# Kernel optimization log

Hardware: AMD Instinct MI355X
Metric: run time of the kernel (lower is better)

The kernel has to match this reference:

```python
import math
import jax, jax.numpy as jnp
import numpy as np

IMAGE_SIZE = 256
RADIUS = 10.0  # radius_list=[10.0] default
EYES_POS_LIST = [[-1, -1, -1], [-1, -1, 1], [-1, 1, -1], [-1, 1, 1],
                 [1, -1, -1], [1, -1, 1], [1, 1, -1], [1, 1, 1]]


def _pre_matrix(view_id):
    # projection_matrix @ look_at(eyes, 0, up=(0,0,1)), orthographic branch
    eyes = np.array(EYES_POS_LIST[view_id], np.float32)  # eyepos_scale=1.0
    ups = np.array([0.0, 0.0, 1.0], np.float32)
    z = eyes / max(float(np.linalg.norm(eyes)), 1e-6)
    x = np.cross(ups, z)
    x = x / max(float(np.linalg.norm(x)), 1e-6)
    y = np.cross(z, x)
    orient = np.eye(4, dtype=np.float32)
    orient[0, :3] = x
    orient[1, :3] = y
    orient[2, :3] = z
    trans = np.eye(4, dtype=np.float32)
    trans[:3, 3] = -eyes
    view = orient @ trans
    z_near, z_far = 0.1, 10.0
    proj = np.diag(np.array([1.5, 1.5, -2.0 / (z_far - z_near), 1.0], np.float32))
    proj[2, 3] = (z_far + z_near) / (z_far - z_near)
    return jnp.asarray((proj @ view).astype(np.float32))


def _p2i_max(pos_ij, feat, batch_inds, background, radius):
    """Splat each point onto its (i,j) pixel footprint with a cos kernel,
    reducing with max (background as init). pos_ij in NDC [-1,1]."""
    B, C, H, W = background.shape  # C == 1
    pts = (pos_ij * 0.5 + 0.5) * jnp.array([H - 1.0, W - 1.0], pos_ij.dtype)  # [P,2] pixel coords
    r = int(math.ceil(radius))
    offs = jnp.arange(-r, r + 2)  # cover full footprint around floor(center)
    di, dj = jnp.meshgrid(offs, offs, indexing="ij")
    di = di.reshape(-1)
    dj = dj.reshape(-1)  # [K], K=(2r+2)^2
    base = jnp.floor(pts).astype(jnp.int32)  # [P,2]
    pi = base[:, :1] + di[None, :]  # [P,K]
    pj = base[:, 1:] + dj[None, :]
    d = jnp.sqrt((pi.astype(pts.dtype) - pts[:, :1]) ** 2 +
                 (pj.astype(pts.dtype) - pts[:, 1:]) ** 2)
    w = jnp.where(d <= radius, jnp.cos(d * (jnp.pi / 2.0 / radius)), 0.0)  # cos kernel
    vals = w * feat  # feat [P,1] broadcasts -> [P,K]
    valid = (pi >= 0) & (pi < H) & (pj >= 0) & (pj < W)
    flat = batch_inds[:, None] * (H * W) + pi * W + pj
    flat = jnp.where(valid, flat, B * H * W)  # dump slot for out-of-bounds
    canvas = jnp.full((B * H * W + 1,), -jnp.inf, background.dtype)
    canvas = canvas.at[flat.reshape(-1)].max(vals.reshape(-1))
    return jnp.maximum(background, canvas[:-1].reshape(B, 1, H, W))


def _forward(data, view_id):
    B, N, _ = data.shape
    M = _pre_matrix(view_id)  # [4,4]
    pcd = data.reshape(-1, 3)  # [B*N,3]
    hom = pcd @ M[:, :3].T + M[:, 3][None, :]  # [B*N,4]
    xyz = hom[:, :3] / hom[:, 3:4]
    pos_ij = jnp.stack([-xyz[:, 1], xyz[:, 0]], axis=1)  # (i,j) = (-y, x)
    z = xyz[:, 2:3]
    feat = 1.0 - (z - z.min()) / (z.max() - z.min())  # [B*N,1]
    batch_inds = jnp.repeat(jnp.arange(B, dtype=jnp.int32), N)
    background = jnp.zeros((B, 1, IMAGE_SIZE, IMAGE_SIZE), data.dtype)
    return _p2i_max(pos_ij, feat, batch_inds, background, RADIUS)


def setup_inputs() -> dict:
    key = jax.random.key(0)
    data = jax.random.normal(key, (32, 4096, 3), dtype=jnp.float32) * 0.5  # unit-ish cloud
    return {"data": data, "view_id": 0}


def reference(data, view_id):
    return _forward(data, view_id)
```

## Files before the change

kernel.cpp:

```cpp
#include <hip/hip_runtime.h>
#include <math.h>

#define IMG_H 256
#define IMG_W 256
#define NBATCH 32
#define NPER 4096
#define NPTS (NBATCH * NPER)
#define STRIP 16
#define NSTRIPS (IMG_H / STRIP)
#define THREADS 1024
#define NWAVES (THREADS / 64)
#define PADL 19
#define ROWW 299
#define CANVAS_W (STRIP * ROWW)
#define KC  0.15707964f
#define KC3 0.47123890f
#define TMAX 2.4674011f
#define BBLK 64
#define CAP 2048


struct Mats { float m[8][12]; };

static void build_mats(float out[8][12]) {
  static const double EYES[8][3] = {
    {-1,-1,-1},{-1,-1, 1},{-1, 1,-1},{-1, 1, 1},
    { 1,-1,-1},{ 1,-1, 1},{ 1, 1,-1},{ 1, 1, 1}};
  for (int v = 0; v < 8; ++v) {
    const double* e = EYES[v];
    double en = sqrt(e[0]*e[0] + e[1]*e[1] + e[2]*e[2]);
    if (en < 1e-6) en = 1e-6;
    double z[3] = {e[0]/en, e[1]/en, e[2]/en};
    double x[3] = {-z[1], z[0], 0.0};
    double xn = sqrt(x[0]*x[0] + x[1]*x[1]);
    if (xn < 1e-6) xn = 1e-6;
    x[0] /= xn; x[1] /= xn; x[2] = 0.0;
    double y[3] = {z[1]*x[2] - z[2]*x[1],
                   z[2]*x[0] - z[0]*x[2],
                   z[0]*x[1] - z[1]*x[0]};
    const double s  = 1.5;
    const double pz = -2.0 / (10.0 - 0.1);
    const double c3 = (10.0 + 0.1) / (10.0 - 0.1);
    double dxe = x[0]*e[0] + x[1]*e[1] + x[2]*e[2];
    double dye = y[0]*e[0] + y[1]*e[1] + y[2]*e[2];
    double dze = z[0]*e[0] + z[1]*e[1] + z[2]*e[2];
    out[v][0] = (float)(s*x[0]); out[v][1] = (float)(s*x[1]);
    out[v][2] = (float)(s*x[2]); out[v][3] = (float)(-s*dxe);
    out[v][4] = (float)(s*y[0]); out[v][5] = (float)(s*y[1]);
    out[v][6] = (float)(s*y[2]); out[v][7] = (float)(-s*dye);
    out[v][8] = (float)(pz*z[0]); out[v][9] = (float)(pz*z[1]);
    out[v][10] = (float)(pz*z[2]); out[v][11] = (float)(-pz*dze + c3);
  }
}

__global__ __launch_bounds__(256)
void zminmax_part(const float* __restrict__ data,
                  const int* __restrict__ view_id,
                  Mats mats, float* __restrict__ red) {
  const int v = (*view_id) & 7;
  const float* M = mats.m[v];
  const float M8 = M[8], M9 = M[9], M10 = M[10], M11 = M[11];
  float zmin = INFINITY, zmax = -INFINITY;
  for (int p = blockIdx.x * blockDim.x + threadIdx.x; p < NPTS;
       p += BBLK * 256) {
    float x = data[3*p+0], y = data[3*p+1], zz = data[3*p+2];
    float z = M8*x + M9*y + M10*zz + M11;
    zmin = fminf(zmin, z);
    zmax = fmaxf(zmax, z);
  }
#pragma unroll
  for (int m = 32; m >= 1; m >>= 1) {
    zmin = fminf(zmin, __shfl_xor(zmin, m, 64));
    zmax = fmaxf(zmax, __shfl_xor(zmax, m, 64));
  }
  __shared__ float smn[4], smx[4];
  if ((threadIdx.x & 63) == 0) {
    smn[threadIdx.x >> 6] = zmin;
    smx[threadIdx.x >> 6] = zmax;
  }
  __syncthreads();
  if (threadIdx.x == 0) {
    float a = fminf(fminf(smn[0], smn[1]), fminf(smn[2], smn[3]));
    float b = fmaxf(fmaxf(smx[0], smx[1]), fmaxf(smx[2], smx[3]));
    red[blockIdx.x] = a;
    red[BBLK + blockIdx.x] = b;
  }
}

__global__ __launch_bounds__(THREADS, 8)
void splat_fused(const float* __restrict__ data,
                 const int* __restrict__ view_id,
                 Mats mats, const float* __restrict__ red,
                 float* __restrict__ out) {
  __shared__ unsigned int canvas[CANVAS_W];
  __shared__ float4 q4[CAP];
  __shared__ int qcnt;
  __shared__ float zred[2];

  const int tid  = threadIdx.x;
  const int lane = tid & 63;
  const int wid  = tid >> 6;
  const int b    = blockIdx.y;
  const int strip = (b < 16) ? (int)blockIdx.x : (15 - (int)blockIdx.x);
  const int si0  = strip * STRIP;

  const int v = (*view_id) & 7;
  const float* M = mats.m[v];
  const float M0 = M[0], M1 = M[1], M2 = M[2],  M3  = M[3];
  const float M4 = M[4], M5 = M[5], M6 = M[6],  M7  = M[7];
  const float M8 = M[8], M9 = M[9], M10 = M[10], M11 = M[11];

  for (int i = tid; i < CANVAS_W; i += THREADS) canvas[i] = 0u;
  if (tid < 64) {
    float a = fminf(red[tid], INFINITY);
    float c = fmaxf(red[BBLK + tid], -INFINITY);
#pragma unroll
    for (int m = 32; m >= 1; m >>= 1) {
      a = fminf(a, __shfl_xor(a, m, 64));
      c = fmaxf(c, __shfl_xor(c, m, 64));
    }
    if (tid == 0) { zred[0] = a; zred[1] = c; qcnt = 0; }
  }
  __syncthreads();

  const float zmin = zred[0];
  const float zinv = 1.0f / (zred[1] - zmin);

  const float2* src2 = (const float2*)(data + (size_t)b * NPER * 3);
#pragma unroll 1
  for (int chunk = 0; chunk < 2; ++chunk) {
    int f2base = chunk * 3072 + 3 * tid;
    float2 A = src2[f2base], Bv = src2[f2base + 1], Cv = src2[f2base + 2];
    float px[2] = {A.x, Bv.y};
    float py[2] = {A.y, Cv.x};
    float pw[2] = {Bv.x, Cv.y};
#pragma unroll
    for (int k = 0; k < 2; ++k) {
      float x = px[k], y = py[k], zz = pw[k];
      float h1 = M4*x + M5*y + M6*zz + M7;
      float pif = (-h1 * 0.5f + 0.5f) * (float)(IMG_H - 1);
      int base_i = (int)floorf(pif);
      int i0 = max(max(base_i - 9, 0), si0);
      int i1 = min(min(base_i + 10, IMG_H - 1), si0 + (STRIP - 1));
      float h0 = M0*x + M1*y + M2*zz + M3;
      float pjf = (h0 * 0.5f + 0.5f) * (float)(IMG_W - 1);
      int base_j = (int)floorf(pjf);
      bool hit = (i0 <= i1) & (base_j >= -10) & (base_j <= IMG_W + 8);

      unsigned long long m = __ballot(hit);
      int cnt = __popcll(m);
      int wbase = 0;
      if (lane == 0 && cnt) wbase = atomicAdd(&qcnt, cnt);
      wbase = __shfl(wbase, 0);
      if (hit) {
        float h2 = M8*x + M9*y + M10*zz + M11;
        float feat = fmaxf(1.0f - (h2 - zmin) * zinv, 0.0f);
        int rows = i1 - i0 + 1;
        int basew = (i0 - si0) * ROWW + (base_j + 10);
        unsigned meta = ((unsigned)rows << 13) | (unsigned)basew;
        float fi_s = ((float)i0 - pif) * KC;
        float fj_s = ((float)(base_j - 9) - pjf) * KC;
        int slot = wbase + (int)__popcll(m & ((1ull << lane) - 1));
        if (slot < CAP)
          q4[slot] = make_float4(fi_s, fj_s, feat, __uint_as_float(meta));
      }
    }
  }
  __syncthreads();

  const int n = min(qcnt, CAP);
  const int r_l   = (lane * 3277) >> 16;
  const int col_l = lane - r_l * 20;
  const float col_kc = (float)col_l * KC;
  const float r_kc   = (float)r_l * KC;

  if (lane < 60) {
    for (int e = wid; e < n; e += NWAVES) {
      float4 Q = q4[e];
      float fi_s = Q.x, fj_s = Q.y, feat = Q.z;
      unsigned meta = __float_as_uint(Q.w);
      int basew = (int)(meta & 0x1FFFu);
      int rows  = (int)(meta >> 13);
      float dy = col_kc + fj_s;
      float dy2 = dy * dy;
      float dx = r_kc + fi_s;
      unsigned int* ptr = canvas + (basew + r_l * ROWW + col_l);
      int rb = 0;
      for (; rb + 3 <= rows; rb += 3) {
        float t = fminf(__builtin_fmaf(dx, dx, dy2), TMAX);
        float w = __builtin_fmaf(t,
                    __builtin_fmaf(t,
                      __builtin_fmaf(t,
                        __builtin_fmaf(t, 2.4801587e-5f, -1.3888889e-3f),
                        4.1666668e-2f),
                      -0.5f),
                    1.0f);
        atomicMax(ptr, __float_as_uint(w * feat));
        dx += KC3;
        ptr += 3 * ROWW;
      }
      if (rb < rows) {
        int row = min(rb + r_l, rows - 1);
        float dxt = __builtin_fmaf((float)row, KC, fi_s);
        float t = fminf(__builtin_fmaf(dxt, dxt, dy2), TMAX);
        float w = __builtin_fmaf(t,
                    __builtin_fmaf(t,
                      __builtin_fmaf(t,
                        __builtin_fmaf(t, 2.4801587e-5f, -1.3888889e-3f),
                        4.1666668e-2f),
                      -0.5f),
                    1.0f);
        atomicMax(canvas + (basew + row * ROWW + col_l),
                  __float_as_uint(w * feat));
      }
    }
  }

  __syncthreads();
  float* outb = out + ((size_t)b * IMG_H + si0) * IMG_W;
#pragma unroll
  for (int i = tid; i < STRIP * IMG_W; i += THREADS) {
    int r = i >> 8, col = i & 255;
    outb[i] = __uint_as_float(canvas[r * ROWW + PADL + col]);
  }
}

extern "C" void kernel_launch(void* const* d_in, const int* in_sizes, int n_in,
                              void* d_out, int out_size, void* d_ws, size_t ws_size,
                              hipStream_t stream) {
  const float* data = (const float*)d_in[0];
  const int* view_id = (const int*)d_in[1];
  float* out = (float*)d_out;
  float* red = (float*)d_ws;

  Mats mats;
  build_mats(mats.m);

  zminmax_part<<<BBLK, 256, 0, stream>>>(data, view_id, mats, red);
  dim3 grid(NSTRIPS, NBATCH);
  splat_fused<<<grid, THREADS, 0, stream>>>(data, view_id, mats, red, out);
}
```

Measured before the change: 34.42 us.

## Fuse z-range reduction into splat kernel using cooperative grid sync

Removes the separate z-min/max kernel. Each of the 512 splat blocks now reduces the z range of 256 points, writes a partial to workspace, and waits on a cooperative-groups grid barrier before every block reduces all partials. This drops one kernel launch and its launch gap. In exchange it adds a grid-wide barrier and requires all 512 blocks of 1024 threads to be co-resident, which the large shared-memory footprint may not allow.

```diff
diff --git a/kernel.cpp b/kernel.cpp
--- a/kernel.cpp
+++ b/kernel.cpp
@@ -1,5 +1,8 @@
 #include <hip/hip_runtime.h>
+#include <hip/hip_cooperative_groups.h>
 #include <math.h>
+
+namespace cg = cooperative_groups;
 
 #define IMG_H 256
 #define IMG_W 256
@@ -10,13 +13,13 @@
 #define NSTRIPS (IMG_H / STRIP)
 #define THREADS 1024
 #define NWAVES (THREADS / 64)
+#define NBLOCKS (NSTRIPS * NBATCH)
 #define PADL 19
 #define ROWW 299
 #define CANVAS_W (STRIP * ROWW)
 #define KC  0.15707964f
 #define KC3 0.47123890f
 #define TMAX 2.4674011f
-#define BBLK 64
 #define CAP 2048
 
 
@@ -53,49 +56,16 @@
   }
 }
 
-__global__ __launch_bounds__(256)
-void zminmax_part(const float* __restrict__ data,
-                  const int* __restrict__ view_id,
-                  Mats mats, float* __restrict__ red) {
-  const int v = (*view_id) & 7;
-  const float* M = mats.m[v];
-  const float M8 = M[8], M9 = M[9], M10 = M[10], M11 = M[11];
-  float zmin = INFINITY, zmax = -INFINITY;
-  for (int p = blockIdx.x * blockDim.x + threadIdx.x; p < NPTS;
-       p += BBLK * 256) {
-    float x = data[3*p+0], y = data[3*p+1], zz = data[3*p+2];
-    float z = M8*x + M9*y + M10*zz + M11;
-    zmin = fminf(zmin, z);
-    zmax = fmaxf(zmax, z);
-  }
-#pragma unroll
-  for (int m = 32; m >= 1; m >>= 1) {
-    zmin = fminf(zmin, __shfl_xor(zmin, m, 64));
-    zmax = fmaxf(zmax, __shfl_xor(zmax, m, 64));
-  }
-  __shared__ float smn[4], smx[4];
-  if ((threadIdx.x & 63) == 0) {
-    smn[threadIdx.x >> 6] = zmin;
-    smx[threadIdx.x >> 6] = zmax;
-  }
-  __syncthreads();
-  if (threadIdx.x == 0) {
-    float a = fminf(fminf(smn[0], smn[1]), fminf(smn[2], smn[3]));
-    float b = fmaxf(fmaxf(smx[0], smx[1]), fmaxf(smx[2], smx[3]));
-    red[blockIdx.x] = a;
-    red[BBLK + blockIdx.x] = b;
-  }
-}
-
 __global__ __launch_bounds__(THREADS, 8)
-void splat_fused(const float* __restrict__ data,
-                 const int* __restrict__ view_id,
-                 Mats mats, const float* __restrict__ red,
-                 float* __restrict__ out) {
+void splat_coop(const float* __restrict__ data,
+                const int* __restrict__ view_id,
+                Mats mats, float* __restrict__ red,
+                float* __restrict__ out) {
   __shared__ unsigned int canvas[CANVAS_W];
   __shared__ float4 q4[CAP];
   __shared__ int qcnt;
   __shared__ float zred[2];
+  __shared__ float smn[4], smx[4];
 
   const int tid  = threadIdx.x;
   const int lane = tid & 63;
@@ -103,6 +73,7 @@
   const int b    = blockIdx.y;
   const int strip = (b < 16) ? (int)blockIdx.x : (15 - (int)blockIdx.x);
   const int si0  = strip * STRIP;
+  const int lin  = (int)blockIdx.y * NSTRIPS + (int)blockIdx.x;
 
   const int v = (*view_id) & 7;
   const float* M = mats.m[v];
@@ -110,10 +81,34 @@
   const float M4 = M[4], M5 = M[5], M6 = M[6],  M7  = M[7];
   const float M8 = M[8], M9 = M[9], M10 = M[10], M11 = M[11];
 
+  if (tid < 256) {
+    const int p = lin * 256 + tid;
+    float x = data[3*p+0], y = data[3*p+1], zz = data[3*p+2];
+    float z = M8*x + M9*y + M10*zz + M11;
+    float zmn = z, zmx = z;
+#pragma unroll
+    for (int m = 32; m >= 1; m >>= 1) {
+      zmn = fminf(zmn, __shfl_xor(zmn, m, 64));
+      zmx = fmaxf(zmx, __shfl_xor(zmx, m, 64));
+    }
+    if (lane == 0) { smn[wid] = zmn; smx[wid] = zmx; }
+  }
+  __syncthreads();
+  if (tid == 0) {
+    red[lin] = fminf(fminf(smn[0], smn[1]), fminf(smn[2], smn[3]));
+    red[NBLOCKS + lin] = fmaxf(fmaxf(smx[0], smx[1]), fmaxf(smx[2], smx[3]));
+  }
+
+  cg::this_grid().sync();
+
   for (int i = tid; i < CANVAS_W; i += THREADS) canvas[i] = 0u;
   if (tid < 64) {
-    float a = fminf(red[tid], INFINITY);
-    float c = fmaxf(red[BBLK + tid], -INFINITY);
+    float a = INFINITY, c = -INFINITY;
+#pragma unroll
+    for (int k = 0; k < NBLOCKS / 64; ++k) {
+      a = fminf(a, red[tid + 64 * k]);
+      c = fmaxf(c, red[NBLOCKS + tid + 64 * k]);
+    }
 #pragma unroll
     for (int m = 32; m >= 1; m >>= 1) {
       a = fminf(a, __shfl_xor(a, m, 64));
@@ -236,7 +231,10 @@
   Mats mats;
   build_mats(mats.m);
 
-  zminmax_part<<<BBLK, 256, 0, stream>>>(data, view_id, mats, red);
   dim3 grid(NSTRIPS, NBATCH);
-  splat_fused<<<grid, THREADS, 0, stream>>>(data, view_id, mats, red, out);
+  dim3 block(THREADS);
+  void* args[] = {(void*)&data, (void*)&view_id, (void*)&mats,
+                  (void*)&red, (void*)&out};
+  hipLaunchCooperativeKernel((const void*)splat_coop, grid, block,
+                             args, 0, stream);
 }
```

Measured after the change: 79.15 us. +130.0%, slower.
